# Kernel optimization log

Measured on AMD Instinct MI355X. Metric: run time of the kernel, lower is better.

Reference implementation:

```python
import jax, jax.numpy as jnp
import numpy as np

N_NODES = 50000
N_EDGES = 800000
N_GRAPHS = 64
NODE_F = 11
EDGE_F = 14
H = 128
P = 128
L = 3
BN_EPS = 1e-5


def setup_inputs() -> dict:
    key = jax.random.key(0)
    ks = jax.random.split(key, 12)
    s = lambda k, sh: (jax.random.normal(k, sh, jnp.float32) * 0.05)
    x = jax.random.normal(ks[0], (N_NODES, NODE_F), jnp.float32)
    edge_index = jax.random.randint(ks[1], (2, N_EDGES), 0, N_NODES)
    edge_attr = jax.random.normal(ks[2], (N_EDGES, EDGE_F), jnp.float32)
    batch_idx = jnp.sort(jax.random.randint(ks[3], (N_NODES,), 0, N_GRAPHS))
    node_W = s(ks[4], (H, NODE_F)); node_b = jnp.zeros((H,), jnp.float32)
    edge_W = s(ks[5], (H, EDGE_F)); edge_b = jnp.zeros((H,), jnp.float32)
    lin1_W = s(ks[6], (L, H, H)); lin1_b = jnp.zeros((L, H), jnp.float32)
    bn_gamma = jnp.ones((L, H), jnp.float32); bn_beta = jnp.zeros((L, H), jnp.float32)
    bn_mean = s(ks[7], (L, H))
    bn_var = jax.random.uniform(ks[8], (L, H), jnp.float32, 0.5, 1.5)
    lin2_W = s(ks[9], (L, H, H)); lin2_b = jnp.zeros((L, H), jnp.float32)
    proj_W = s(ks[10], (P, H)); proj_b = jnp.zeros((P,), jnp.float32)
    return dict(x=x, edge_index=edge_index, edge_attr=edge_attr, batch_idx=batch_idx,
                node_W=node_W, node_b=node_b, edge_W=edge_W, edge_b=edge_b,
                lin1_W=lin1_W, lin1_b=lin1_b, bn_gamma=bn_gamma, bn_beta=bn_beta,
                bn_mean=bn_mean, bn_var=bn_var, lin2_W=lin2_W, lin2_b=lin2_b,
                proj_W=proj_W, proj_b=proj_b)


def reference(x, edge_index, edge_attr, batch_idx, node_W, node_b, edge_W, edge_b,
              lin1_W, lin1_b, bn_gamma, bn_beta, bn_mean, bn_var,
              lin2_W, lin2_b, proj_W, proj_b):
    src, dst = edge_index[0], edge_index[1]
    h = x @ node_W.T + node_b            # [N, H] node embedding
    e = edge_attr @ edge_W.T + edge_b    # [E, H] edge embedding
    for i in range(L):
        # GINEConv: out = MLP((1+eps)*h + sum_j ReLU(h_j + e_ij)), eps = 0
        msg = jax.nn.relu(h[src] + e)                              # [E, H]
        agg = jax.ops.segment_sum(msg, dst, num_segments=N_NODES)  # [N, H]
        z = h + agg
        z = z @ lin1_W[i].T + lin1_b[i]
        # BatchNorm1d in eval mode (running stats)
        z = (z - bn_mean[i]) * (bn_gamma[i] * jax.lax.rsqrt(bn_var[i] + BN_EPS)) + bn_beta[i]
        z = jax.nn.relu(z)
        z = z @ lin2_W[i].T + lin2_b[i]
        # encoder: relu -> dropout(eval, identity) -> residual add
        h = jax.nn.relu(z) + h
    # global_mean_pool over graphs in the batch
    ones = jnp.ones((N_NODES,), h.dtype)
    counts = jax.ops.segment_sum(ones, batch_idx, num_segments=N_GRAPHS)
    pooled = jax.ops.segment_sum(h, batch_idx, num_segments=N_GRAPHS)
    pooled = pooled / jnp.maximum(counts, 1.0)[:, None]            # [G, H]
    return pooled @ proj_W.T + proj_b                              # [G, P]
```

## Files before the change

kernel.cpp:

```cpp
#include <hip/hip_runtime.h>

typedef unsigned int uint;
typedef unsigned short ushort;
typedef __attribute__((ext_vector_type(8))) short bf16x8;
typedef __attribute__((ext_vector_type(4))) float f32x4;
typedef __attribute__((ext_vector_type(2))) _Float16 half2_t;

#define NN 50000
#define NE 800000
#define NG 64
#define NODE_F 11
#define EDGE_F 14
#define HD 128
#define NL 3
#define BN_EPS 1e-5f

#if defined(__has_builtin)
#if __has_builtin(__builtin_amdgcn_fdot2)
#define HAS_DOT2 1
#endif
#endif

__device__ __forceinline__ uint bfround(float v) {
    uint b = __float_as_uint(v);
    return (b + 0x7fffu + ((b >> 16) & 1u)) >> 16;
}

__device__ __forceinline__ float dot2f(half2_t a, half2_t b, float acc) {
#ifdef HAS_DOT2
    return __builtin_amdgcn_fdot2(a, b, acc, false);
#else
    return acc + (float)a[0] * (float)b[0] + (float)a[1] * (float)b[1];
#endif
}

__device__ __forceinline__ half2_t u2h2(uint u) {
    return __builtin_bit_cast(half2_t, u);
}

__global__ __launch_bounds__(256)
void init_kernel(const float* __restrict__ x, const float* __restrict__ nW,
                 const float* __restrict__ nb_, const float* __restrict__ lin1,
                 const float* __restrict__ lin2, const float* __restrict__ proj,
                 const float* __restrict__ ea, const int2* __restrict__ pairs,
                 uint* __restrict__ hb, uint* __restrict__ ea_h,
                 int* __restrict__ srcs, ushort* __restrict__ wb,
                 float* __restrict__ projT)
{
    int bid = blockIdx.x;
    if (bid < 448) {
        int idx = bid * 256 + threadIdx.x;
        if (idx < 6 * HD * HD) {
            int m = idx >> 14, e = idx & (HD * HD - 1);
            const float* src = (m < 3) ? (lin1 + m * HD * HD) : (lin2 + (m - 3) * HD * HD);
            wb[idx] = (ushort)bfround(src[e]);
        } else if (idx < 7 * HD * HD) {
            int e = idx - 6 * HD * HD;
            int r = e >> 7, c = e & 127;
            projT[c * HD + r] = proj[r * HD + c];
        }
    } else if (bid < 448 + 12500) {
        uint idx = (uint)(bid - 448) * 256u + threadIdx.x;
        uint node = idx >> 6, cp = idx & 63u;
        uint c2 = cp * 2u;
        const float* xr = x + node * NODE_F;
        const float* w0 = nW + c2 * NODE_F;
        const float* w1 = w0 + NODE_F;
        float a0 = nb_[c2], a1 = nb_[c2 + 1];
#pragma unroll
        for (int f = 0; f < NODE_F; ++f) { float xv = xr[f]; a0 += xv * w0[f]; a1 += xv * w1[f]; }
        hb[idx] = bfround(a0) | (bfround(a1) << 16);
    } else if (bid < 448 + 12500 + 25000) {
        uint idx = (uint)(bid - 448 - 12500) * 256u + threadIdx.x;
        uint el = idx >> 3, f2 = idx & 7u;
        if (f2 >= 7u) return;
        float2 v = *(const float2*)(ea + (size_t)pairs[el].y * EDGE_F + 2 * f2);
        half2_t hh;
        hh[0] = (_Float16)v.x;
        hh[1] = (_Float16)v.y;
        ea_h[el * 7u + f2] = __builtin_bit_cast(uint, hh);
    } else {
        uint i = (uint)(bid - 448 - 12500 - 25000) * 256u + threadIdx.x;
        if (i < NE) srcs[i] = pairs[i].x;
    }
}

__global__ __launch_bounds__(256)
void hist_kernel(const int* __restrict__ ei, int* __restrict__ deg)
{
    int e = blockIdx.x * 256 + threadIdx.x;
    if (e < NE) atomicAdd(&deg[ei[NE + e]], 1);
}

__global__ __launch_bounds__(256)
void scan1_kernel(const int* __restrict__ deg, int* __restrict__ incl, int* __restrict__ bsum)
{
    int i = blockIdx.x * 256 + threadIdx.x;
    int v = (i < NN) ? deg[i] : 0;
    int lane = threadIdx.x & 63;
#pragma unroll
    for (int off = 1; off < 64; off <<= 1) {
        int u = __shfl_up(v, off);
        if (lane >= off) v += u;
    }
    __shared__ int wsum[4];
    if (lane == 63) wsum[threadIdx.x >> 6] = v;
    __syncthreads();
    int wid = threadIdx.x >> 6;
    int add = 0;
#pragma unroll
    for (int w = 0; w < 3; ++w) if (w < wid) add += wsum[w];
    v += add;
    if (i < NN) incl[i] = v;
    if (threadIdx.x == 255) bsum[blockIdx.x] = v;
}

__global__ __launch_bounds__(256)
void scan2_kernel(const int* __restrict__ bsum, int* __restrict__ bscan, int nb)
{
    int i = threadIdx.x;
    int v = (i < nb) ? bsum[i] : 0;
    int lane = i & 63;
#pragma unroll
    for (int off = 1; off < 64; off <<= 1) {
        int u = __shfl_up(v, off);
        if (lane >= off) v += u;
    }
    __shared__ int wsum[4];
    if (lane == 63) wsum[i >> 6] = v;
    __syncthreads();
    int wid = i >> 6;
    int add = 0;
#pragma unroll
    for (int w = 0; w < 3; ++w) if (w < wid) add += wsum[w];
    v += add;
    bscan[i] = v;
}

__global__ __launch_bounds__(256)
void scan3_kernel(const int* __restrict__ deg, const int* __restrict__ incl,
                  const int* __restrict__ bscan, int* __restrict__ row_start,
                  int* __restrict__ cursor)
{
    int i = blockIdx.x * 256 + threadIdx.x;
    if (i >= NN) return;
    int b = blockIdx.x;
    int base = (b > 0) ? bscan[b - 1] : 0;
    int rs = base + incl[i] - deg[i];
    row_start[i] = rs;
    cursor[i] = rs;
    if (i == 0) row_start[NN] = NE;
}

__global__ __launch_bounds__(256)
void scatter_kernel(const int* __restrict__ ei, int* __restrict__ cursor,
                    int2* __restrict__ pairs)
{
    int e = blockIdx.x * 256 + threadIdx.x;
    if (e >= NE) return;
    int s = ei[e], d = ei[NE + e];
    int pos = atomicAdd(&cursor[d], 1);
    pairs[pos] = make_int2(s, e);
}

#define EMSGH(HV, EP)                                                       \
    {                                                                       \
        float ax = bx, ay = by;                                             \
        _Pragma("unroll")                                                   \
        for (int f = 0; f < 7; ++f) {                                       \
            half2_t av = u2h2((EP)[f]);                                     \
            ax = dot2f(av, w0h[f], ax);                                     \
            ay = dot2f(av, w1h[f], ay);                                     \
        }                                                                   \
        float hx = __uint_as_float((HV) << 16);                             \
        float hy = __uint_as_float((HV) & 0xffff0000u);                     \
        accx += fmaxf(hx + ax, 0.f);                                        \
        accy += fmaxf(hy + ay, 0.f);                                        \
    }

__global__ __launch_bounds__(256)
void agg_f16_kernel(const uint* __restrict__ hb,
                    const int* __restrict__ srcs, const int* __restrict__ row_start,
                    const uint* __restrict__ ea_h, const float* __restrict__ eW,
                    const float* __restrict__ eb, uint* __restrict__ zin_b)
{
    uint node = blockIdx.x * 4u + (threadIdx.x >> 6);
    if (node >= NN) return;
    uint lane = threadIdx.x & 63u;
    uint c2 = lane * 2u;
    const float4* wp = (const float4*)(eW + lane * 28u);
    float4 q0 = wp[0], q1 = wp[1], q2 = wp[2], q3 = wp[3], q4 = wp[4], q5 = wp[5], q6 = wp[6];
    half2_t w0h[7], w1h[7];
    w0h[0][0]=(_Float16)q0.x; w0h[0][1]=(_Float16)q0.y;
    w0h[1][0]=(_Float16)q0.z; w0h[1][1]=(_Float16)q0.w;
    w0h[2][0]=(_Float16)q1.x; w0h[2][1]=(_Float16)q1.y;
    w0h[3][0]=(_Float16)q1.z; w0h[3][1]=(_Float16)q1.w;
    w0h[4][0]=(_Float16)q2.x; w0h[4][1]=(_Float16)q2.y;
    w0h[5][0]=(_Float16)q2.z; w0h[5][1]=(_Float16)q2.w;
    w0h[6][0]=(_Float16)q3.x; w0h[6][1]=(_Float16)q3.y;
    w1h[0][0]=(_Float16)q3.z; w1h[0][1]=(_Float16)q3.w;
    w1h[1][0]=(_Float16)q4.x; w1h[1][1]=(_Float16)q4.y;
    w1h[2][0]=(_Float16)q4.z; w1h[2][1]=(_Float16)q4.w;
    w1h[3][0]=(_Float16)q5.x; w1h[3][1]=(_Float16)q5.y;
    w1h[4][0]=(_Float16)q5.z; w1h[4][1]=(_Float16)q5.w;
    w1h[5][0]=(_Float16)q6.x; w1h[5][1]=(_Float16)q6.y;
    w1h[6][0]=(_Float16)q6.z; w1h[6][1]=(_Float16)q6.w;
    float bx = eb[c2], by = eb[c2 + 1];
    float accx = 0.f, accy = 0.f;
    int beg = __builtin_amdgcn_readfirstlane(row_start[node]);
    int end = __builtin_amdgcn_readfirstlane(row_start[node + 1]);
    int j = beg;
    for (; j + 8 <= end; j += 8) {
        uint s[8];
        uint hv[8];
#pragma unroll
        for (int q = 0; q < 8; ++q) s[q] = (uint)srcs[(uint)j + q];
#pragma unroll
        for (int q = 0; q < 8; ++q) hv[q] = hb[s[q] * 64u + lane];
        const uint* e0 = ea_h + (uint)j * 7u;
        EMSGH(hv[0], e0);      EMSGH(hv[1], e0 + 7);
        EMSGH(hv[2], e0 + 14); EMSGH(hv[3], e0 + 21);
        EMSGH(hv[4], e0 + 28); EMSGH(hv[5], e0 + 35);
        EMSGH(hv[6], e0 + 42); EMSGH(hv[7], e0 + 49);
    }
    for (; j + 4 <= end; j += 4) {
        uint s0 = (uint)srcs[(uint)j], s1 = (uint)srcs[(uint)j + 1];
        uint s2 = (uint)srcs[(uint)j + 2], s3 = (uint)srcs[(uint)j + 3];
        uint hv0 = hb[s0 * 64u + lane];
        uint hv1 = hb[s1 * 64u + lane];
        uint hv2 = hb[s2 * 64u + lane];
        uint hv3 = hb[s3 * 64u + lane];
        const uint* e0 = ea_h + (uint)j * 7u;
        EMSGH(hv0, e0);      EMSGH(hv1, e0 + 7);
        EMSGH(hv2, e0 + 14); EMSGH(hv3, e0 + 21);
    }
    for (; j < end; ++j) {
        uint hv0 = hb[(uint)srcs[(uint)j] * 64u + lane];
        const uint* e0 = ea_h + (uint)j * 7u;
        EMSGH(hv0, e0);
    }
    uint hself = hb[node * 64u + lane];
    accx += __uint_as_float(hself << 16);
    accy += __uint_as_float(hself & 0xffff0000u);
    zin_b[node * 64u + lane] = bfround(accx) | (bfround(accy) << 16);
}

__global__ __launch_bounds__(256)
void fused_layer_kernel(const uint* __restrict__ zin_b,
                        const ushort* __restrict__ w1b, const float* __restrict__ b1,
                        const float* __restrict__ gamma, const float* __restrict__ beta,
                        const float* __restrict__ mean, const float* __restrict__ var,
                        const ushort* __restrict__ w2b, const float* __restrict__ b2,
                        ushort* __restrict__ hb, int n)
{
    __shared__ uint Ahi[64 * 64];
    const int t = threadIdx.x;
    const int nb = blockIdx.x * 64;

    {
        int row = t >> 2;
        int kq = (t & 3) * 16;
        int gn = nb + row;
        uint vals[16];
        if (gn < n) {
            const uint4* src = (const uint4*)(zin_b + (size_t)gn * 64 + kq);
#pragma unroll
            for (int i = 0; i < 4; ++i) {
                uint4 v = src[i];
                vals[4 * i] = v.x; vals[4 * i + 1] = v.y; vals[4 * i + 2] = v.z; vals[4 * i + 3] = v.w;
            }
        } else {
#pragma unroll
            for (int i = 0; i < 16; ++i) vals[i] = 0;
        }
        uint rowbase = row * 256;
#pragma unroll
        for (int i = 0; i < 4; ++i) {
            uint byte = (rowbase + (kq + 4 * i) * 4) ^ ((row & 7) << 4);
            *(uint4*)((char*)Ahi + byte) = make_uint4(vals[4 * i], vals[4 * i + 1], vals[4 * i + 2], vals[4 * i + 3]);
        }
    }

    const int w  = t >> 6, l = t & 63;
    const int lc = l & 15, lk = l >> 4;
    bf16x8 wf1[2][4], wf2[2][4];
#pragma unroll
    for (int ct = 0; ct < 2; ++ct)
#pragma unroll
        for (int ks = 0; ks < 4; ++ks) {
            size_t off = (size_t)(w * 32 + ct * 16 + lc) * HD + ks * 32 + lk * 8;
            wf1[ct][ks] = *(const bf16x8*)(w1b + off);
            wf2[ct][ks] = *(const bf16x8*)(w2b + off);
        }

    __syncthreads();

    f32x4 acc[4][2];
#pragma unroll
    for (int rt = 0; rt < 4; ++rt)
#pragma unroll
        for (int ct = 0; ct < 2; ++ct) acc[rt][ct] = (f32x4){0.f, 0.f, 0.f, 0.f};

#pragma unroll
    for (int ks = 0; ks < 4; ++ks) {
#pragma unroll
        for (int rt = 0; rt < 4; ++rt) {
            int row = rt * 16 + lc;
            uint byte = ((uint)(row * 256 + (ks * 32 + lk * 8) * 2)) ^ ((row & 7) << 4);
            bf16x8 ah = *(const bf16x8*)((char*)Ahi + byte);
            acc[rt][0] = __builtin_amdgcn_mfma_f32_16x16x32_bf16(ah, wf1[0][ks], acc[rt][0], 0, 0, 0);
            acc[rt][1] = __builtin_amdgcn_mfma_f32_16x16x32_bf16(ah, wf1[1][ks], acc[rt][1], 0, 0, 0);
        }
    }

    __syncthreads();

#pragma unroll
    for (int ct = 0; ct < 2; ++ct) {
        int col = w * 32 + ct * 16 + lc;
        float bi = b1[col];
        float scv = gamma[col] * rsqrtf(var[col] + BN_EPS);
        float shv = beta[col] - mean[col] * scv;
#pragma unroll
        for (int rt = 0; rt < 4; ++rt) {
#pragma unroll
            for (int r = 0; r < 4; ++r) {
                int rowl = rt * 16 + lk * 4 + r;
                float v = (acc[rt][ct][r] + bi) * scv + shv;
                v = fmaxf(v, 0.f);
                uint byte = ((uint)(rowl * 256 + col * 2)) ^ ((rowl & 7) << 4);
                *(ushort*)((char*)Ahi + byte) = (ushort)bfround(v);
            }
        }
    }

    __syncthreads();

    f32x4 acc2[4][2];
#pragma unroll
    for (int rt = 0; rt < 4; ++rt)
#pragma unroll
        for (int ct = 0; ct < 2; ++ct) acc2[rt][ct] = (f32x4){0.f, 0.f, 0.f, 0.f};

#pragma unroll
    for (int ks = 0; ks < 4; ++ks) {
#pragma unroll
        for (int rt = 0; rt < 4; ++rt) {
            int row = rt * 16 + lc;
            uint byte = ((uint)(row * 256 + (ks * 32 + lk * 8) * 2)) ^ ((row & 7) << 4);
            bf16x8 az = *(const bf16x8*)((char*)Ahi + byte);
            acc2[rt][0] = __builtin_amdgcn_mfma_f32_16x16x32_bf16(az, wf2[0][ks], acc2[rt][0], 0, 0, 0);
            acc2[rt][1] = __builtin_amdgcn_mfma_f32_16x16x32_bf16(az, wf2[1][ks], acc2[rt][1], 0, 0, 0);
        }
    }

#pragma unroll
    for (int ct = 0; ct < 2; ++ct) {
        int col = w * 32 + ct * 16 + lc;
        float bi = b2[col];
#pragma unroll
        for (int rt = 0; rt < 4; ++rt) {
#pragma unroll
            for (int r = 0; r < 4; ++r) {
                int row = nb + rt * 16 + lk * 4 + r;
                if (row < n) {
                    float hprev = __uint_as_float(((uint)hb[(size_t)row * HD + col]) << 16);
                    float v = fmaxf(acc2[rt][ct][r] + bi, 0.f) + hprev;
                    hb[(size_t)row * HD + col] = (ushort)bfround(v);
                }
            }
        }
    }
}

__global__ __launch_bounds__(128)
void pool_kernel(const ushort* __restrict__ hb, const int* __restrict__ batch,
                 float* __restrict__ pooled, int* __restrict__ counts, int n, int chunk)
{
    int c = threadIdx.x;
    int n_start = blockIdx.x * chunk;
    if (n_start >= n) return;
    int n_end = min(n_start + chunk, n);
    float local = 0.f;
    int cnt = 0;
    int g_cur = batch[n_start];
    for (int nd = n_start; nd < n_end; ++nd) {
        int g = batch[nd];
        if (g != g_cur) {
            atomicAdd(&pooled[g_cur * HD + c], local);
            if (c == 0) atomicAdd(&counts[g_cur], cnt);
            local = 0.f; cnt = 0; g_cur = g;
        }
        local += __uint_as_float(((uint)hb[(size_t)nd * HD + c]) << 16);
        cnt++;
    }
    atomicAdd(&pooled[g_cur * HD + c], local);
    if (c == 0) atomicAdd(&counts[g_cur], cnt);
}

__global__ __launch_bounds__(128)
void final_kernel(const float* __restrict__ pooled, const int* __restrict__ counts,
                  const float* __restrict__ projT, const float* __restrict__ pb,
                  float* __restrict__ out)
{
    __shared__ float p_lds[HD];
    int g = blockIdx.x, p = threadIdx.x;
    float inv = 1.f / fmaxf((float)counts[g], 1.f);
    p_lds[p] = pooled[g * HD + p];
    __syncthreads();
    float acc = 0.f;
#pragma unroll 4
    for (int c = 0; c < HD; ++c) acc += p_lds[c] * projT[c * HD + p];
    out[g * HD + p] = acc * inv + pb[p];
}

extern "C" void kernel_launch(void* const* d_in, const int* in_sizes, int n_in,
                              void* d_out, int out_size, void* d_ws, size_t ws_size,
                              hipStream_t stream)
{
    const float* x        = (const float*)d_in[0];
    const int*   edge_idx = (const int*)d_in[1];
    const float* edge_attr= (const float*)d_in[2];
    const int*   batch    = (const int*)d_in[3];
    const float* node_W   = (const float*)d_in[4];
    const float* node_b   = (const float*)d_in[5];
    const float* edge_W   = (const float*)d_in[6];
    const float* edge_b   = (const float*)d_in[7];
    const float* lin1_b   = (const float*)d_in[9];
    const float* bn_gamma = (const float*)d_in[10];
    const float* bn_beta  = (const float*)d_in[11];
    const float* bn_mean  = (const float*)d_in[12];
    const float* bn_var   = (const float*)d_in[13];
    const float* lin2_b   = (const float*)d_in[15];
    const float* proj_b   = (const float*)d_in[17];

    char* ws = (char*)d_ws;
    uint*   hb       = (uint*)  (ws);
    uint*   zin_b    = (uint*)  (ws + 12800000);
    uint*   ea_h     = (uint*)  (ws + 25600000);
    int2*   pairs    = (int2*)  (ws + 48000000);
    int*    srcs     = (int*)   (ws + 54400000);
    ushort* wb       = (ushort*)(ws + 57600000);
    float*  projT    = (float*) (ws + 57800000);
    float*  pooled   = (float*) (ws + 57900000);
    int*    counts   = (int*)   (ws + 57932768);
    int*    deg      = (int*)   (ws + 57940000);
    int*    incl     = (int*)   (ws + 58140000);
    int*    bsum     = (int*)   (ws + 58340000);
    int*    bscan    = (int*)   (ws + 58342048);
    int*    row_start= (int*)   (ws + 58344096);
    int*    cursor   = (int*)   (ws + 58544160);

    const int NB = (NN + 255) / 256;

    hipMemsetAsync(deg, 0, NN * sizeof(int), stream);
    hist_kernel<<<(NE + 255) / 256, 256, 0, stream>>>(edge_idx, deg);
    scan1_kernel<<<NB, 256, 0, stream>>>(deg, incl, bsum);
    scan2_kernel<<<1, 256, 0, stream>>>(bsum, bscan, NB);
    scan3_kernel<<<NB, 256, 0, stream>>>(deg, incl, bscan, row_start, cursor);
    scatter_kernel<<<(NE + 255) / 256, 256, 0, stream>>>(edge_idx, cursor, pairs);

    init_kernel<<<448 + 12500 + 25000 + 3125, 256, 0, stream>>>(
        x, node_W, node_b, (const float*)d_in[8], (const float*)d_in[14],
        (const float*)d_in[16], edge_attr, pairs, hb, ea_h, srcs, wb, projT);

    for (int i = 0; i < NL; ++i) {
        agg_f16_kernel<<<(NN + 3) / 4, 256, 0, stream>>>(
            hb, srcs, row_start, ea_h, edge_W, edge_b, zin_b);
        fused_layer_kernel<<<(NN + 63) / 64, 256, 0, stream>>>(
            zin_b, wb + (size_t)i * HD * HD, lin1_b + i * HD,
            bn_gamma + i * HD, bn_beta + i * HD, bn_mean + i * HD, bn_var + i * HD,
            wb + (size_t)(3 + i) * HD * HD, lin2_b + i * HD,
            (ushort*)hb, NN);
    }

    hipMemsetAsync(pooled, 0, NG * HD * sizeof(float) + NG * sizeof(int) + 4000, stream);
    pool_kernel<<<(NN + 31) / 32, 128, 0, stream>>>((const ushort*)hb, batch, pooled, counts, NN, 32);
    final_kernel<<<NG, HD, 0, stream>>>(pooled, counts, projT, proj_b, (float*)d_out);
}
```

Measured before the change: 403.8 us.

## Pack source index and f16 edge features into 32-byte CSR edge records

```diff
diff --git a/kernel.cpp b/kernel.cpp
--- a/kernel.cpp
+++ b/kernel.cpp
@@ -42,9 +42,7 @@
 void init_kernel(const float* __restrict__ x, const float* __restrict__ nW,
                  const float* __restrict__ nb_, const float* __restrict__ lin1,
                  const float* __restrict__ lin2, const float* __restrict__ proj,
-                 const float* __restrict__ ea, const int2* __restrict__ pairs,
-                 uint* __restrict__ hb, uint* __restrict__ ea_h,
-                 int* __restrict__ srcs, ushort* __restrict__ wb,
+                 uint* __restrict__ hb, ushort* __restrict__ wb,
                  float* __restrict__ projT)
 {
     int bid = blockIdx.x;
@@ -59,7 +57,7 @@
             int r = e >> 7, c = e & 127;
             projT[c * HD + r] = proj[r * HD + c];
         }
-    } else if (bid < 448 + 12500) {
+    } else {
         uint idx = (uint)(bid - 448) * 256u + threadIdx.x;
         uint node = idx >> 6, cp = idx & 63u;
         uint c2 = cp * 2u;
@@ -70,18 +68,6 @@
 #pragma unroll
         for (int f = 0; f < NODE_F; ++f) { float xv = xr[f]; a0 += xv * w0[f]; a1 += xv * w1[f]; }
         hb[idx] = bfround(a0) | (bfround(a1) << 16);
-    } else if (bid < 448 + 12500 + 25000) {
-        uint idx = (uint)(bid - 448 - 12500) * 256u + threadIdx.x;
-        uint el = idx >> 3, f2 = idx & 7u;
-        if (f2 >= 7u) return;
-        float2 v = *(const float2*)(ea + (size_t)pairs[el].y * EDGE_F + 2 * f2);
-        half2_t hh;
-        hh[0] = (_Float16)v.x;
-        hh[1] = (_Float16)v.y;
-        ea_h[el * 7u + f2] = __builtin_bit_cast(uint, hh);
-    } else {
-        uint i = (uint)(bid - 448 - 12500 - 25000) * 256u + threadIdx.x;
-        if (i < NE) srcs[i] = pairs[i].x;
     }
 }
 
@@ -153,14 +139,26 @@
 }
 
 __global__ __launch_bounds__(256)
-void scatter_kernel(const int* __restrict__ ei, int* __restrict__ cursor,
-                    int2* __restrict__ pairs)
+void scatter_kernel(const int* __restrict__ ei, const float* __restrict__ ea,
+                    int* __restrict__ cursor, uint* __restrict__ erec)
 {
     int e = blockIdx.x * 256 + threadIdx.x;
     if (e >= NE) return;
     int s = ei[e], d = ei[NE + e];
+    uint f[7];
+    const float2* er = (const float2*)(ea + (size_t)e * EDGE_F);
+#pragma unroll
+    for (int i = 0; i < 7; ++i) {
+        float2 v = er[i];
+        half2_t hh;
+        hh[0] = (_Float16)v.x;
+        hh[1] = (_Float16)v.y;
+        f[i] = __builtin_bit_cast(uint, hh);
+    }
     int pos = atomicAdd(&cursor[d], 1);
-    pairs[pos] = make_int2(s, e);
+    uint* dst = erec + (size_t)pos * 8;
+    *(uint4*)dst = make_uint4((uint)s, f[0], f[1], f[2]);
+    *(uint4*)(dst + 4) = make_uint4(f[3], f[4], f[5], f[6]);
 }
 
 #define EMSGH(HV, EP)                                                       \
@@ -179,9 +177,8 @@
     }
 
 __global__ __launch_bounds__(256)
-void agg_f16_kernel(const uint* __restrict__ hb,
-                    const int* __restrict__ srcs, const int* __restrict__ row_start,
-                    const uint* __restrict__ ea_h, const float* __restrict__ eW,
+void agg_f16_kernel(const uint* __restrict__ hb, const uint* __restrict__ erec,
+                    const int* __restrict__ row_start, const float* __restrict__ eW,
                     const float* __restrict__ eb, uint* __restrict__ zin_b)
 {
     uint node = blockIdx.x * 4u + (threadIdx.x >> 6);
@@ -211,33 +208,32 @@
     int end = __builtin_amdgcn_readfirstlane(row_start[node + 1]);
     int j = beg;
     for (; j + 8 <= end; j += 8) {
+        const uint* r0 = erec + (uint)j * 8u;
         uint s[8];
         uint hv[8];
 #pragma unroll
-        for (int q = 0; q < 8; ++q) s[q] = (uint)srcs[(uint)j + q];
+        for (int q = 0; q < 8; ++q) s[q] = r0[q * 8];
 #pragma unroll
         for (int q = 0; q < 8; ++q) hv[q] = hb[s[q] * 64u + lane];
-        const uint* e0 = ea_h + (uint)j * 7u;
-        EMSGH(hv[0], e0);      EMSGH(hv[1], e0 + 7);
-        EMSGH(hv[2], e0 + 14); EMSGH(hv[3], e0 + 21);
-        EMSGH(hv[4], e0 + 28); EMSGH(hv[5], e0 + 35);
-        EMSGH(hv[6], e0 + 42); EMSGH(hv[7], e0 + 49);
+        EMSGH(hv[0], r0 + 1);  EMSGH(hv[1], r0 + 9);
+        EMSGH(hv[2], r0 + 17); EMSGH(hv[3], r0 + 25);
+        EMSGH(hv[4], r0 + 33); EMSGH(hv[5], r0 + 41);
+        EMSGH(hv[6], r0 + 49); EMSGH(hv[7], r0 + 57);
     }
     for (; j + 4 <= end; j += 4) {
-        uint s0 = (uint)srcs[(uint)j], s1 = (uint)srcs[(uint)j + 1];
-        uint s2 = (uint)srcs[(uint)j + 2], s3 = (uint)srcs[(uint)j + 3];
+        const uint* r0 = erec + (uint)j * 8u;
+        uint s0 = r0[0], s1 = r0[8], s2 = r0[16], s3 = r0[24];
         uint hv0 = hb[s0 * 64u + lane];
         uint hv1 = hb[s1 * 64u + lane];
         uint hv2 = hb[s2 * 64u + lane];
         uint hv3 = hb[s3 * 64u + lane];
-        const uint* e0 = ea_h + (uint)j * 7u;
-        EMSGH(hv0, e0);      EMSGH(hv1, e0 + 7);
-        EMSGH(hv2, e0 + 14); EMSGH(hv3, e0 + 21);
+        EMSGH(hv0, r0 + 1);  EMSGH(hv1, r0 + 9);
+        EMSGH(hv2, r0 + 17); EMSGH(hv3, r0 + 25);
     }
     for (; j < end; ++j) {
-        uint hv0 = hb[(uint)srcs[(uint)j] * 64u + lane];
-        const uint* e0 = ea_h + (uint)j * 7u;
-        EMSGH(hv0, e0);
+        const uint* r0 = erec + (uint)j * 8u;
+        uint hv0 = hb[r0[0] * 64u + lane];
+        EMSGH(hv0, r0 + 1);
     }
     uint hself = hb[node * 64u + lane];
     accx += __uint_as_float(hself << 16);
@@ -437,19 +433,17 @@
     char* ws = (char*)d_ws;
     uint*   hb       = (uint*)  (ws);
     uint*   zin_b    = (uint*)  (ws + 12800000);
-    uint*   ea_h     = (uint*)  (ws + 25600000);
-    int2*   pairs    = (int2*)  (ws + 48000000);
-    int*    srcs     = (int*)   (ws + 54400000);
-    ushort* wb       = (ushort*)(ws + 57600000);
-    float*  projT    = (float*) (ws + 57800000);
-    float*  pooled   = (float*) (ws + 57900000);
-    int*    counts   = (int*)   (ws + 57932768);
-    int*    deg      = (int*)   (ws + 57940000);
-    int*    incl     = (int*)   (ws + 58140000);
-    int*    bsum     = (int*)   (ws + 58340000);
-    int*    bscan    = (int*)   (ws + 58342048);
-    int*    row_start= (int*)   (ws + 58344096);
-    int*    cursor   = (int*)   (ws + 58544160);
+    uint*   erec     = (uint*)  (ws + 25600000);
+    ushort* wb       = (ushort*)(ws + 51200000);
+    float*  projT    = (float*) (ws + 51400000);
+    float*  pooled   = (float*) (ws + 51500000);
+    int*    counts   = (int*)   (ws + 51532768);
+    int*    deg      = (int*)   (ws + 51540000);
+    int*    incl     = (int*)   (ws + 51740000);
+    int*    bsum     = (int*)   (ws + 51940000);
+    int*    bscan    = (int*)   (ws + 51942048);
+    int*    row_start= (int*)   (ws + 51944096);
+    int*    cursor   = (int*)   (ws + 52144160);
 
     const int NB = (NN + 255) / 256;
 
@@ -458,15 +452,15 @@
     scan1_kernel<<<NB, 256, 0, stream>>>(deg, incl, bsum);
     scan2_kernel<<<1, 256, 0, stream>>>(bsum, bscan, NB);
     scan3_kernel<<<NB, 256, 0, stream>>>(deg, incl, bscan, row_start, cursor);
-    scatter_kernel<<<(NE + 255) / 256, 256, 0, stream>>>(edge_idx, cursor, pairs);
-
-    init_kernel<<<448 + 12500 + 25000 + 3125, 256, 0, stream>>>(
+    scatter_kernel<<<(NE + 255) / 256, 256, 0, stream>>>(edge_idx, edge_attr, cursor, erec);
+
+    init_kernel<<<448 + 12500, 256, 0, stream>>>(
         x, node_W, node_b, (const float*)d_in[8], (const float*)d_in[14],
-        (const float*)d_in[16], edge_attr, pairs, hb, ea_h, srcs, wb, projT);
+        (const float*)d_in[16], hb, wb, projT);
 
     for (int i = 0; i < NL; ++i) {
         agg_f16_kernel<<<(NN + 3) / 4, 256, 0, stream>>>(
-            hb, srcs, row_start, ea_h, edge_W, edge_b, zin_b);
+            hb, erec, row_start, edge_W, edge_b, zin_b);
         fused_layer_kernel<<<(NN + 63) / 64, 256, 0, stream>>>(
             zin_b, wb + (size_t)i * HD * HD, lin1_b + i * HD,
             bn_gamma + i * HD, bn_beta + i * HD, bn_mean + i * HD, bn_var + i * HD,
```

Result: faster. 370.5 us (-8.2%).
